# Kernel optimization log

Measured on AMD Instinct MI355X. Metric: run time of the kernel, lower is better.

Reference implementation:

```python
import jax, jax.numpy as jnp
import numpy as np

N = 200          # fixed by map_norm's .view(200, 1)
D = 8192         # in_features
EPS = 1e-5


def setup_inputs() -> dict:
    key = jax.random.key(0)
    ks = jax.random.split(key, 7)
    lim = float(np.sqrt(6.0 / D))
    x = jax.random.normal(ks[0], (N, D), dtype=jnp.float32)
    Wq = jax.random.uniform(ks[1], (D, D), dtype=jnp.float32, minval=-lim, maxval=lim)
    Wk = jax.random.uniform(ks[2], (D, D), dtype=jnp.float32, minval=-lim, maxval=lim)
    Wv = jax.random.uniform(ks[3], (D, D), dtype=jnp.float32, minval=-lim, maxval=lim)
    bq = jax.random.normal(ks[4], (D,), dtype=jnp.float32) * 0.01
    bk = jax.random.normal(ks[5], (D,), dtype=jnp.float32) * 0.01
    bv = jax.random.normal(ks[6], (D,), dtype=jnp.float32) * 0.01
    return {"x": x, "Wq": Wq, "bq": bq, "Wk": Wk, "bk": bk, "Wv": Wv, "bv": bv}


def reference(x, Wq, bq, Wk, bk, Wv, bv):
    d_out = x.shape[1]
    cc = jnp.sqrt(jnp.asarray(d_out, dtype=x.dtype))
    # nn.Linear: y = x @ W.T + b
    q = x @ Wq.T + bq          # [N, D]
    k = x @ Wk.T + bk          # [N, D]
    v = x @ Wv.T + bv          # [N, D]
    s = q @ k.T                # [N, N] score map
    mean = jnp.mean(s, axis=-1, keepdims=True)
    var = jnp.var(s, axis=-1, keepdims=True, ddof=1)  # torch.var is unbiased
    s = (s - mean) / jnp.sqrt(var + EPS)
    s = jnp.sin(s)
    scores = jax.nn.softmax(s / cc, axis=-1)
    return scores @ v          # [N, D]
```

## Files before the change

kernel.cpp:

```cpp
#include <hip/hip_runtime.h>
#include <hip/hip_bf16.h>
#include <cstdint>

#define DD 8192
#define NROW 200
#define MT 13
#define MPAD 208
#define KPV 256
#define EPSV 1e-5f
#define BK 64
#define ABUF_BYTES (MPAD * BK * 2)

using short8 = __attribute__((ext_vector_type(8))) short;
using f32x4  = __attribute__((ext_vector_type(4))) float;

__device__ __forceinline__ ushort f2bf(float f) {
    union { float f; unsigned u; } c; c.f = f;
    unsigned u = c.u;
    return (ushort)((u + 0x7FFFu + ((u >> 16) & 1u)) >> 16);
}

__device__ __forceinline__ short8 pack8(float4 a, float4 b) {
    short8 o;
    o[0]=f2bf(a.x); o[1]=f2bf(a.y); o[2]=f2bf(a.z); o[3]=f2bf(a.w);
    o[4]=f2bf(b.x); o[5]=f2bf(b.y); o[6]=f2bf(b.z); o[7]=f2bf(b.w);
    return o;
}

__device__ __forceinline__ short8 pack8f(f32x4 a, f32x4 b) {
    short8 o;
    union { __hip_bfloat162 h; unsigned u; } q;
    q.h = __float22bfloat162_rn(float2{a[0], a[1]}); o[0]=(short)(q.u & 0xffff); o[1]=(short)(q.u >> 16);
    q.h = __float22bfloat162_rn(float2{a[2], a[3]}); o[2]=(short)(q.u & 0xffff); o[3]=(short)(q.u >> 16);
    q.h = __float22bfloat162_rn(float2{b[0], b[1]}); o[4]=(short)(q.u & 0xffff); o[5]=(short)(q.u >> 16);
    q.h = __float22bfloat162_rn(float2{b[2], b[3]}); o[6]=(short)(q.u & 0xffff); o[7]=(short)(q.u >> 16);
    return o;
}

__global__ void cvt_x(const float* __restrict__ x, ushort* __restrict__ xb) {
    int i = (blockIdx.x * 256 + threadIdx.x) * 8;
    int row = i >> 13;
    int col = i & (DD - 1);
    short8 o;
    if (row < NROW) {
        const float4* p = reinterpret_cast<const float4*>(x + (size_t)row * DD + col);
        float4 a = p[0], b = p[1];
        o = pack8(a, b);
    } else {
        for (int j = 0; j < 8; ++j) o[j] = 0;
    }
    *reinterpret_cast<short8*>(xb + i) = o;
}

#define GL(dst, ptr, OFF) \
    asm volatile("global_load_dwordx4 %0, %1, off offset:" #OFF \
                 : "=&v"(dst) : "v"(ptr) : "memory")
#define WAITV(N) asm volatile("s_waitcnt vmcnt(" #N ")" ::: "memory")
#define SB __builtin_amdgcn_sched_barrier(0)
#define RAWBAR asm volatile("s_barrier" ::: "memory")

__global__ __launch_bounds__(384) void qkv_s6(
    const ushort* __restrict__ xb,
    const float* __restrict__ Wq, const float* __restrict__ Wk, const float* __restrict__ Wv,
    const float* __restrict__ bq, const float* __restrict__ bk, const float* __restrict__ bv,
    ushort* __restrict__ qb, ushort* __restrict__ kb, ushort* __restrict__ vt)
{
    __shared__ char L[2 * ABUF_BYTES];

    const int cb   = blockIdx.x;
    const int t    = threadIdx.x;
    const int lane = t & 63;
    const int wave = t >> 6;
    const int mat  = wave >> 1;
    const int cg   = wave & 1;
    const int c    = lane & 15;
    const int kgrp = lane >> 4;
    const int ncol = cb * 32 + cg * 16 + c;

    const float* W    = (mat == 0) ? Wq : (mat == 1 ? Wk : Wv);
    const float* bias = (mat == 0) ? bq : (mat == 1 ? bk : bv);
    const float* wq   = W + (size_t)ncol * DD + kgrp * 8;

    const ushort* sbase = xb + (size_t)(lane >> 3) * DD
                             + (size_t)(((lane & 7) ^ ((lane >> 3) & 7)) * 8);

    const int b0off = c * 128 + ((kgrp ^ (c & 7)) * 16);
    const int b1off = b0off ^ 64;

    f32x4 acc[MT];
    #pragma unroll
    for (int m = 0; m < MT; ++m)
        for (int r = 0; r < 4; ++r) acc[m][r] = 0.f;

    f32x4 uA0, uA1, uA2, uA3, uB0, uB1, uB2, uB3;

#define STAGE(B, KK) { _Pragma("unroll") for (int j = 0; j < 5; ++j) { \
        int g = wave + 6 * j; \
        if (g < 26) { \
            __builtin_amdgcn_global_load_lds( \
                (const __attribute__((address_space(1))) void*)(sbase + (KK) + (size_t)g * 8 * DD), \
                (__attribute__((address_space(3))) void*)(L + (B) + g * 1024), \
                16, 0, 0); } } }

#define COMPUTE(RB, bb0, bb1) { _Pragma("unroll") for (int m = 0; m < MT; ++m) { \
        short8 a0 = *reinterpret_cast<const short8*>(L + (RB) + m * 2048 + b0off); \
        acc[m] = __builtin_amdgcn_mfma_f32_16x16x32_bf16(a0, bb0, acc[m], 0, 0, 0); \
        short8 a1 = *reinterpret_cast<const short8*>(L + (RB) + m * 2048 + b1off); \
        acc[m] = __builtin_amdgcn_mfma_f32_16x16x32_bf16(a1, bb1, acc[m], 0, 0, 0); } }

#define PHASE(RB, UC) { \
        STAGE((RB) ^ ABUF_BYTES, kn); \
        kn = (kn + BK) & (DD - 1); \
        if (wave < 2) { WAITV(9); } else { WAITV(8); } \
        SB; \
        short8 bb0 = pack8f(UC##0, UC##1); \
        short8 bb1 = pack8f(UC##2, UC##3); \
        GL(UC##0, wq + k2, 0); \
        GL(UC##1, wq + k2, 16); \
        GL(UC##2, wq + k2, 128); \
        GL(UC##3, wq + k2, 144); \
        k2 = (k2 + BK) & (DD - 1); \
        RAWBAR; \
        COMPUTE(RB, bb0, bb1); \
        asm volatile("s_waitcnt lgkmcnt(0)" ::: "memory"); \
        RAWBAR; }

    int kn = BK;
    int k2 = 2 * BK;
    STAGE(0, 0);
    GL(uA0, wq, 0);  GL(uA1, wq, 16);  GL(uA2, wq, 128);  GL(uA3, wq, 144);
    GL(uB0, wq + BK, 0); GL(uB1, wq + BK, 16); GL(uB2, wq + BK, 128); GL(uB3, wq + BK, 144);

    #pragma unroll 1
    for (int it = 0; it < DD / (2 * BK); ++it) {
        PHASE(0, uA);
        PHASE(ABUF_BYTES, uB);
    }
#undef PHASE
#undef COMPUTE
#undef STAGE

    const float bv0 = bias[ncol];
    if (mat < 2) {
        ushort* outb = (mat == 0) ? qb : kb;
        #pragma unroll
        for (int m = 0; m < MT; ++m)
            for (int r = 0; r < 4; ++r) {
                int row = m * 16 + kgrp * 4 + r;
                outb[(size_t)row * DD + ncol] = f2bf(acc[m][r] + bv0);
            }
    } else {
        #pragma unroll
        for (int m = 0; m < MT; ++m)
            for (int r = 0; r < 4; ++r) {
                int row = m * 16 + kgrp * 4 + r;
                vt[(size_t)ncol * KPV + row] = f2bf(acc[m][r] + bv0);
            }
    }
}

__global__ __launch_bounds__(256) void sgemm(const ushort* __restrict__ qb, const ushort* __restrict__ kb,
                                             float* __restrict__ sbuf) {
    const int bm = blockIdx.y, bn = blockIdx.x;
    const int lane  = threadIdx.x & 63;
    const int wave  = threadIdx.x >> 6;
    const int col16 = lane & 15, kgrp = lane >> 4;
    const ushort* ap = qb + (size_t)(bm * 16 + col16) * DD + kgrp * 8;
    const ushort* bp = kb + (size_t)(bn * 16 + col16) * DD + kgrp * 8;
    f32x4 acc;
    for (int r = 0; r < 4; ++r) acc[r] = 0.f;
    const int kend = (wave + 1) * 2048;
    for (int k0 = wave * 2048; k0 < kend; k0 += 32) {
        short8 a = *reinterpret_cast<const short8*>(ap + k0);
        short8 b = *reinterpret_cast<const short8*>(bp + k0);
        acc = __builtin_amdgcn_mfma_f32_16x16x32_bf16(a, b, acc, 0, 0, 0);
    }
    __shared__ f32x4 red[4][64];
    red[wave][lane] = acc;
    __syncthreads();
    if (wave == 0) {
        f32x4 s = red[0][lane];
        for (int j = 1; j < 4; ++j) { f32x4 o = red[j][lane]; for (int r = 0; r < 4; ++r) s[r] += o[r]; }
        for (int r = 0; r < 4; ++r)
            sbuf[(size_t)(bm * 16 + kgrp * 4 + r) * MPAD + bn * 16 + col16] = s[r];
    }
}

__global__ __launch_bounds__(256) void rownorm(const float* __restrict__ sbuf, ushort* __restrict__ pb) {
    const int row = blockIdx.x;
    const int t = threadIdx.x;
    if (row >= NROW) { pb[(size_t)row * KPV + t] = 0; return; }
    __shared__ float part[4];
    const int lane = t & 63, wave = t >> 6;
    float x = (t < NROW) ? sbuf[(size_t)row * MPAD + t] : 0.f;

    float s = x;
    for (int m = 32; m; m >>= 1) s += __shfl_xor(s, m, 64);
    if (lane == 0) part[wave] = s;
    __syncthreads();
    float mean = (part[0] + part[1] + part[2] + part[3]) * (1.f / 200.f);

    float d = (t < NROW) ? (x - mean) : 0.f;
    float s2 = d * d;
    for (int m = 32; m; m >>= 1) s2 += __shfl_xor(s2, m, 64);
    __syncthreads();
    if (lane == 0) part[wave] = s2;
    __syncthreads();
    float var = (part[0] + part[1] + part[2] + part[3]) * (1.f / 199.f);

    float inv = 1.f / sqrtf(var + EPSV);
    float y = sinf(d * inv);
    const float inv_cc = 1.f / 90.50966799187809f;
    float e = (t < NROW) ? expf(y * inv_cc) : 0.f;

    float se = e;
    for (int m = 32; m; m >>= 1) se += __shfl_xor(se, m, 64);
    __syncthreads();
    if (lane == 0) part[wave] = se;
    __syncthreads();
    float tot = part[0] + part[1] + part[2] + part[3];
    pb[(size_t)row * KPV + t] = (t < NROW) ? f2bf(e / tot) : (ushort)0;
}

__global__ __launch_bounds__(256) void pv_gemm(const ushort* __restrict__ pb, const ushort* __restrict__ vt,
                                               float* __restrict__ out) {
    const int lane  = threadIdx.x & 63;
    const int wave  = threadIdx.x >> 6;
    const int col16 = lane & 15, kgrp = lane >> 4;
    const int ncol  = blockIdx.x * 64 + wave * 16 + col16;
    const ushort* ap = pb + (size_t)col16 * KPV + kgrp * 8;
    const ushort* bp = vt + (size_t)ncol  * KPV + kgrp * 8;
    f32x4 acc[MT];
    for (int m = 0; m < MT; ++m)
        for (int r = 0; r < 4; ++r) acc[m][r] = 0.f;
    for (int k0 = 0; k0 < KPV; k0 += 32) {
        short8 b = *reinterpret_cast<const short8*>(bp + k0);
        #pragma unroll
        for (int m = 0; m < MT; ++m) {
            short8 a = *reinterpret_cast<const short8*>(ap + (size_t)m * 16 * KPV + k0);
            acc[m] = __builtin_amdgcn_mfma_f32_16x16x32_bf16(a, b, acc[m], 0, 0, 0);
        }
    }
    for (int m = 0; m < MT; ++m)
        for (int r = 0; r < 4; ++r) {
            int row = m * 16 + kgrp * 4 + r;
            if (row < NROW) out[(size_t)row * DD + ncol] = acc[m][r];
        }
}

extern "C" void kernel_launch(void* const* d_in, const int* in_sizes, int n_in,
                              void* d_out, int out_size, void* d_ws, size_t ws_size,
                              hipStream_t stream) {
    const float* x  = (const float*)d_in[0];
    const float* Wq = (const float*)d_in[1];
    const float* bq = (const float*)d_in[2];
    const float* Wk = (const float*)d_in[3];
    const float* bk = (const float*)d_in[4];
    const float* Wv = (const float*)d_in[5];
    const float* bv = (const float*)d_in[6];
    float* out = (float*)d_out;

    char* ws = (char*)d_ws;
    ushort* xb   = (ushort*)(ws);
    ushort* qb   = (ushort*)(ws + 3407872);
    ushort* kb   = (ushort*)(ws + 6815744);
    ushort* vt   = (ushort*)(ws + 10223616);
    float*  sbuf = (float*)(ws + 14417920);
    ushort* pb   = (ushort*)(ws + 14590976);

    cvt_x<<<832, 256, 0, stream>>>(x, xb);
    qkv_s6<<<256, 384, 0, stream>>>(xb, Wq, Wk, Wv, bq, bk, bv, qb, kb, vt);
    sgemm<<<dim3(13, 13), 256, 0, stream>>>(qb, kb, sbuf);
    rownorm<<<208, 256, 0, stream>>>(sbuf, pb);
    pv_gemm<<<128, 256, 0, stream>>>(pb, vt, out);
}
```

Measured before the change: 254.8 us.

## Split QKV projection M-tiles across twice as many waves per block

The QKV projection kernel now launches 12 waves per block instead of 6. Each pair of waves shares the same weight columns but splits the 13 M-tiles into two halves of 7; the middle tile is computed by both waves, and only one of them writes it. Only the first six waves stage activations into LDS, and a final wait plus barrier is added before the epilogue. The aim is more waves to hide memory latency and fewer accumulator registers per wave. The cost is that each weight column is fetched twice from global memory, plus some redundant MFMA work.

```diff
diff --git a/kernel.cpp b/kernel.cpp
--- a/kernel.cpp
+++ b/kernel.cpp
@@ -9,6 +9,7 @@
 #define KPV 256
 #define EPSV 1e-5f
 #define BK 64
+#define MT7 7
 #define ABUF_BYTES (MPAD * BK * 2)
 
 using short8 = __attribute__((ext_vector_type(8))) short;
@@ -59,7 +60,7 @@
 #define SB __builtin_amdgcn_sched_barrier(0)
 #define RAWBAR asm volatile("s_barrier" ::: "memory")
 
-__global__ __launch_bounds__(384) void qkv_s6(
+__global__ __launch_bounds__(768) void qkv_w12(
     const ushort* __restrict__ xb,
     const float* __restrict__ Wq, const float* __restrict__ Wk, const float* __restrict__ Wv,
     const float* __restrict__ bq, const float* __restrict__ bk, const float* __restrict__ bv,
@@ -71,8 +72,9 @@
     const int t    = threadIdx.x;
     const int lane = t & 63;
     const int wave = t >> 6;
-    const int mat  = wave >> 1;
-    const int cg   = wave & 1;
+    const int mat  = wave >> 2;
+    const int cg   = (wave >> 1) & 1;
+    const int mh   = wave & 1;
     const int c    = lane & 15;
     const int kgrp = lane >> 4;
     const int ncol = cb * 32 + cg * 16 + c;
@@ -87,31 +89,34 @@
     const int b0off = c * 128 + ((kgrp ^ (c & 7)) * 16);
     const int b1off = b0off ^ 64;
 
-    f32x4 acc[MT];
+    f32x4 acc[MT7];
     #pragma unroll
-    for (int m = 0; m < MT; ++m)
+    for (int m = 0; m < MT7; ++m)
         for (int r = 0; r < 4; ++r) acc[m][r] = 0.f;
 
     f32x4 uA0, uA1, uA2, uA3, uB0, uB1, uB2, uB3;
 
-#define STAGE(B, KK) { _Pragma("unroll") for (int j = 0; j < 5; ++j) { \
+#define STAGE(B, KK) { if (wave < 6) { _Pragma("unroll") for (int j = 0; j < 5; ++j) { \
         int g = wave + 6 * j; \
         if (g < 26) { \
             __builtin_amdgcn_global_load_lds( \
                 (const __attribute__((address_space(1))) void*)(sbase + (KK) + (size_t)g * 8 * DD), \
                 (__attribute__((address_space(3))) void*)(L + (B) + g * 1024), \
-                16, 0, 0); } } }
-
-#define COMPUTE(RB, bb0, bb1) { _Pragma("unroll") for (int m = 0; m < MT; ++m) { \
-        short8 a0 = *reinterpret_cast<const short8*>(L + (RB) + m * 2048 + b0off); \
+                16, 0, 0); } } } }
+
+#define COMPUTE(RB, bb0, bb1) { _Pragma("unroll") for (int m = 0; m < MT7; ++m) { \
+        int tt = mh * 6 + m; \
+        short8 a0 = *reinterpret_cast<const short8*>(L + (RB) + tt * 2048 + b0off); \
         acc[m] = __builtin_amdgcn_mfma_f32_16x16x32_bf16(a0, bb0, acc[m], 0, 0, 0); \
-        short8 a1 = *reinterpret_cast<const short8*>(L + (RB) + m * 2048 + b1off); \
+        short8 a1 = *reinterpret_cast<const short8*>(L + (RB) + tt * 2048 + b1off); \
         acc[m] = __builtin_amdgcn_mfma_f32_16x16x32_bf16(a1, bb1, acc[m], 0, 0, 0); } }
 
 #define PHASE(RB, UC) { \
         STAGE((RB) ^ ABUF_BYTES, kn); \
         kn = (kn + BK) & (DD - 1); \
-        if (wave < 2) { WAITV(9); } else { WAITV(8); } \
+        if (wave >= 6)     { WAITV(4); } \
+        else if (wave < 2) { WAITV(9); } \
+        else               { WAITV(8); } \
         SB; \
         short8 bb0 = pack8f(UC##0, UC##1); \
         short8 bb1 = pack8f(UC##2, UC##3); \
@@ -140,22 +145,33 @@
 #undef COMPUTE
 #undef STAGE
 
+    asm volatile("s_waitcnt vmcnt(0) lgkmcnt(0)" ::: "memory");
+    RAWBAR;
+
     const float bv0 = bias[ncol];
     if (mat < 2) {
         ushort* outb = (mat == 0) ? qb : kb;
         #pragma unroll
-        for (int m = 0; m < MT; ++m)
-            for (int r = 0; r < 4; ++r) {
-                int row = m * 16 + kgrp * 4 + r;
-                outb[(size_t)row * DD + ncol] = f2bf(acc[m][r] + bv0);
+        for (int m = 0; m < MT7; ++m) {
+            if (m >= mh) {
+                #pragma unroll
+                for (int r = 0; r < 4; ++r) {
+                    int row = (mh * 6 + m) * 16 + kgrp * 4 + r;
+                    outb[(size_t)row * DD + ncol] = f2bf(acc[m][r] + bv0);
+                }
             }
+        }
     } else {
         #pragma unroll
-        for (int m = 0; m < MT; ++m)
-            for (int r = 0; r < 4; ++r) {
-                int row = m * 16 + kgrp * 4 + r;
-                vt[(size_t)ncol * KPV + row] = f2bf(acc[m][r] + bv0);
+        for (int m = 0; m < MT7; ++m) {
+            if (m >= mh) {
+                #pragma unroll
+                for (int r = 0; r < 4; ++r) {
+                    int row = (mh * 6 + m) * 16 + kgrp * 4 + r;
+                    vt[(size_t)ncol * KPV + row] = f2bf(acc[m][r] + bv0);
+                }
             }
+        }
     }
 }
 
@@ -269,7 +285,7 @@
     ushort* pb   = (ushort*)(ws + 14590976);
 
     cvt_x<<<832, 256, 0, stream>>>(x, xb);
-    qkv_s6<<<256, 384, 0, stream>>>(xb, Wq, Wk, Wv, bq, bk, bv, qb, kb, vt);
+    qkv_w12<<<256, 768, 0, stream>>>(xb, Wq, Wk, Wv, bq, bk, bv, qb, kb, vt);
     sgemm<<<dim3(13, 13), 256, 0, stream>>>(qb, kb, sbuf);
     rownorm<<<208, 256, 0, stream>>>(sbuf, pb);
     pv_gemm<<<128, 256, 0, stream>>>(pb, vt, out);
```

After: 288.1 us. 13.0% more time.
